# Kernel tuning notes

Hardware: AMD Instinct MI355X
Metric: run time of the kernel (lower is better)

Reference implementation:

```python
import jax, jax.numpy as jnp
import numpy as np

B, S, D, H = 4, 2048, 1024, 16
DK = D // H


def setup_inputs() -> dict:
    key = jax.random.key(0)
    ks = jax.random.split(key, 10)
    std = 0.02
    inp = {
        "input": jax.random.normal(ks[0], (B, S, D), dtype=jnp.float32),
        "attention_reweight": jax.random.uniform(ks[1], (B, S), dtype=jnp.float32),
        "mask": 1,
        "Wq": jax.random.normal(ks[2], (D, D), dtype=jnp.float32) * std,
        "bq": jnp.zeros((D,), dtype=jnp.float32),
        "Wk": jax.random.normal(ks[3], (D, D), dtype=jnp.float32) * std,
        "bk": jnp.zeros((D,), dtype=jnp.float32),
        "Wv": jax.random.normal(ks[4], (D, D), dtype=jnp.float32) * std,
        "bv": jnp.zeros((D,), dtype=jnp.float32),
        "Wo": jax.random.normal(ks[5], (D, D), dtype=jnp.float32) * std,
        "bo": jnp.zeros((D,), dtype=jnp.float32),
    }
    return inp


def reference(input, attention_reweight, mask, Wq, bq, Wk, bk, Wv, bv, Wo, bo):
    b, s, d = input.shape
    # QKV projections (torch Linear: x @ W.T + b)
    q = (input @ Wq.T + bq).reshape(b, s, H, DK).transpose(0, 2, 1, 3)  # [B,H,S,dk]
    k = (input @ Wk.T + bk).reshape(b, s, H, DK).transpose(0, 2, 1, 3)
    v = (input @ Wv.T + bv).reshape(b, s, H, DK).transpose(0, 2, 1, 3)

    scores = jnp.einsum("bhqd,bhkd->bhqk", q, k)  # [B,H,S,S]
    if mask:
        causal = jnp.triu(jnp.ones((s, s), dtype=scores.dtype), k=1)
        scores = scores - causal * 1e9
    scores = scores / jnp.sqrt(jnp.asarray(DK, dtype=jnp.float32))
    # reweight per key position: [B,S] broadcast over heads and query positions
    scores = scores * attention_reweight[:, None, None, :]

    attn = jax.nn.softmax(scores, axis=-1)
    out = jnp.einsum("bhqk,bhkd->bhqd", attn, v)  # [B,H,S,dk]
    out = out.transpose(0, 2, 1, 3).reshape(b, s, d)
    return out @ Wo.T + bo
```

## Files before the change

### kernel.cpp

```cpp
#include <hip/hip_runtime.h>
#include <math.h>

#define B_  4
#define S_  2048
#define D_  1024
#define H_  16
#define DK_ 64

typedef __bf16 bf16x8 __attribute__((ext_vector_type(8)));
typedef float  f32x4  __attribute__((ext_vector_type(4)));

__device__ __forceinline__ unsigned short f2bf(float f) {
  unsigned int u = __builtin_bit_cast(unsigned int, f);
  u += 0x7fffu + ((u >> 16) & 1u);
  return (unsigned short)(u >> 16);
}

__device__ __forceinline__ unsigned short bfbits(float f) {
  __bf16 h = (__bf16)f;
  return __builtin_bit_cast(unsigned short, h);
}

__device__ __forceinline__ f32x4 mfma16(bf16x8 a, bf16x8 b, f32x4 c) {
  return __builtin_amdgcn_mfma_f32_16x16x32_bf16(a, b, c, 0, 0, 0);
}

__device__ __forceinline__ void gl_lds16(const unsigned short* g, unsigned short* l) {
  __builtin_amdgcn_global_load_lds(
      (const __attribute__((address_space(1))) void*)g,
      (__attribute__((address_space(3))) void*)l, 16, 0, 0);
}

__global__ void SAA_cast_all(const float* __restrict__ x,
                             const float* __restrict__ s1, const float* __restrict__ s2,
                             const float* __restrict__ s3, const float* __restrict__ s4,
                             unsigned short* __restrict__ dx,
                             unsigned short* __restrict__ d1, unsigned short* __restrict__ d2,
                             unsigned short* __restrict__ d3, unsigned short* __restrict__ d4)
{
  const int y = blockIdx.y;
  const float* src = (y == 0) ? x : (y == 1) ? s1 : (y == 2) ? s2 : (y == 3) ? s3 : s4;
  unsigned short* dst = (y == 0) ? dx : (y == 1) ? d1 : (y == 2) ? d2 : (y == 3) ? d3 : d4;
  const int n4 = (y == 0) ? (B_ * S_ * D_) / 4 : (D_ * D_) / 4;
  int i = blockIdx.x * blockDim.x + threadIdx.x;
  int stride = gridDim.x * blockDim.x;
  for (; i < n4; i += stride) {
    float4 v = reinterpret_cast<const float4*>(src)[i];
    ushort4 o;
    o.x = f2bf(v.x); o.y = f2bf(v.y); o.z = f2bf(v.z); o.w = f2bf(v.w);
    reinterpret_cast<ushort4*>(dst)[i] = o;
  }
}

__global__ __launch_bounds__(512)
void SAA_gemm_qkv(const unsigned short* __restrict__ Xb,
                  const unsigned short* __restrict__ Wqb,
                  const unsigned short* __restrict__ Wkb,
                  const unsigned short* __restrict__ Wvb,
                  const float* __restrict__ bq,
                  const float* __restrict__ bk,
                  const float* __restrict__ bv,
                  const float* __restrict__ rw,
                  unsigned short* __restrict__ Qo,
                  unsigned short* __restrict__ Ko,
                  unsigned short* __restrict__ Vto)
{
  const int K = D_;
  __shared__ __attribute__((aligned(16))) unsigned short smem[65536];
#define sAp(sl)     (smem + (sl) * 8192)
#define sBp(sl, m)  (smem + 16384 + ((sl) * 3 + (m)) * 8192)

  const int t = threadIdx.x;
  const int w = t >> 6, l = t & 63;
  const int wm = w >> 2, wn = w & 3;
  const int lr = l & 15, lg = l >> 4;
  const int r7 = lr & 7;

  const int bid = blockIdx.x;
  const int m0 = (bid >> 3) * 128;
  const int n0 = (bid & 7) * 128;

  const unsigned short* gA  = Xb  + (size_t)m0 * K;
  const unsigned short* gB0 = Wqb + (size_t)n0 * K;
  const unsigned short* gB1 = Wkb + (size_t)n0 * K;
  const unsigned short* gB2 = Wvb + (size_t)n0 * K;

  int srow[2], soff[2];
#pragma unroll
  for (int i = 0; i < 2; i++) {
    const int c = i * 512 + t;
    srow[i] = c >> 3;
    soff[i] = ((c & 7) ^ (srow[i] & 7)) * 8;
  }

#define STAGE(s, k0)                                                          \
  do {                                                                        \
    _Pragma("unroll")                                                         \
    for (int i = 0; i < 2; i++) {                                             \
      const size_t go = (size_t)srow[i] * K + (k0) + soff[i];                 \
      const int dl = (i * 512 + t) * 8;                                       \
      gl_lds16(gA  + go, sAp(s) + dl);                                        \
      gl_lds16(gB0 + go, sBp(s, 0) + dl);                                     \
      gl_lds16(gB1 + go, sBp(s, 1) + dl);                                     \
      gl_lds16(gB2 + go, sBp(s, 2) + dl);                                     \
    }                                                                         \
  } while (0)

  STAGE(0, 0);

  f32x4 acc[3][4][2] = {};

#pragma unroll 2
  for (int T = 0; T < 16; ++T) {
    __syncthreads();
    if (T + 1 < 16) STAGE((T + 1) & 1, (T + 1) * 64);

    const unsigned short* At = sAp(T & 1);
#pragma unroll
    for (int ks = 0; ks < 2; ++ks) {
      const int swk = (((ks * 4 + lg) ^ r7) << 3);
      bf16x8 afr[4];
#pragma unroll
      for (int mi = 0; mi < 4; ++mi)
        afr[mi] = *reinterpret_cast<const bf16x8*>(
            &At[(wm * 64 + mi * 16 + lr) * 64 + swk]);
#pragma unroll
      for (int mat = 0; mat < 3; ++mat) {
        const unsigned short* Bt = sBp(T & 1, mat);
        bf16x8 bfr[2];
#pragma unroll
        for (int n = 0; n < 2; ++n)
          bfr[n] = *reinterpret_cast<const bf16x8*>(
              &Bt[(wn * 32 + n * 16 + lr) * 64 + swk]);
#pragma unroll
        for (int mi = 0; mi < 4; ++mi)
#pragma unroll
          for (int n = 0; n < 2; ++n)
            acc[mat][mi][n] = mfma16(afr[mi], bfr[n], acc[mat][mi][n]);
      }
    }
  }
#undef STAGE

  __syncthreads();

#pragma unroll
  for (int n = 0; n < 2; ++n) {
    const int col = n0 + wn * 32 + n * 16 + lr;
    const int h = col >> 6, dk = col & 63;
    const float bvv = bv[col];
#pragma unroll
    for (int mi = 0; mi < 4; ++mi) {
      const int row0 = m0 + wm * 64 + mi * 16 + lg * 4;
      const int b = row0 >> 11, s0 = row0 & 2047;
      ushort4 pk;
      pk.x = bfbits(acc[2][mi][n][0] + bvv);
      pk.y = bfbits(acc[2][mi][n][1] + bvv);
      pk.z = bfbits(acc[2][mi][n][2] + bvv);
      pk.w = bfbits(acc[2][mi][n][3] + bvv);
      *reinterpret_cast<ushort4*>(
          &Vto[(((size_t)b * H_ + h) * DK_ + dk) * S_ + s0]) = pk;
    }
  }

  unsigned short* bounce = smem;
  for (int mat = 0; mat < 2; ++mat) {
    const float* bias = mat ? bk : bq;
#pragma unroll
    for (int n = 0; n < 2; ++n) {
      const int col = n0 + wn * 32 + n * 16 + lr;
      const int lcol = wn * 32 + n * 16 + lr;
      const float bs = bias[col];
#pragma unroll
      for (int mi = 0; mi < 4; ++mi) {
#pragma unroll
        for (int r = 0; r < 4; ++r) {
          const int lrow = wm * 64 + mi * 16 + lg * 4 + r;
          float v = acc[mat][mi][n][r] + bs;
          if (mat) v *= 0.18033688011112042f * rw[m0 + lrow];
          bounce[lrow * 132 + lcol] = bfbits(v);
        }
      }
    }
    __syncthreads();
#pragma unroll
    for (int i = 0; i < 2; ++i) {
      const int idx = i * 512 + t;
      const int lrow = idx >> 3, c16 = (idx & 7) * 16;
      const int row = m0 + lrow;
      const int b = row >> 11, s = row & 2047;
      const int col = n0 + c16;
      const int h = col >> 6, dk = col & 63;
      const unsigned short* srcp = &bounce[lrow * 132 + c16];
      unsigned short* dst = (mat ? Ko : Qo) + (((size_t)b * H_ + h) * S_ + s) * DK_ + dk;
#pragma unroll
      for (int j = 0; j < 4; ++j)
        reinterpret_cast<ushort4*>(dst)[j] =
            reinterpret_cast<const ushort4*>(srcp)[j];
    }
    __syncthreads();
  }
#undef sAp
#undef sBp
}

__global__ __launch_bounds__(512)
void SAA_attn(const unsigned short* __restrict__ Q,
              const unsigned short* __restrict__ Kb,
              const unsigned short* __restrict__ Vt,
              const int* __restrict__ maskp,
              unsigned short* __restrict__ Cb)
{
  const int L = (blockIdx.x & 7) * 64 + (blockIdx.x >> 3);
  const int pairid = L & 7;
  const int h = (L >> 3) & 15;
  const int b = L >> 7;

  const int t = threadIdx.x, w = t >> 6, l = t & 63;
  const int lr = l & 15, lg = l >> 4;
  const int mask = maskp[0];

  __shared__ __attribute__((aligned(16))) unsigned short Kt[2][64 * 64];
  __shared__ __attribute__((aligned(16))) unsigned short Vl[2][64 * 64];
  __shared__ __attribute__((aligned(16))) unsigned short Pl[8][16 * 64];

  const size_t bh = (size_t)b * H_ + h;
  const unsigned short* Qbh = Q + bh * S_ * DK_;
  const unsigned short* Kbh = Kb + bh * S_ * DK_;
  const unsigned short* Vbh = Vt + bh * DK_ * S_;
  unsigned short* Pw = &Pl[w][0];

  const int r0 = t >> 3, cc0 = t & 7;
  const int sw0 = (cc0 ^ (r0 & 7)) * 8;

  for (int half = 0; half < 2; ++half) {
    const int qb = half ? (15 - pairid) : pairid;
    const int q0 = qb * 128;
    const int wq = q0 + w * 16;

    bf16x8 qf[2];
#pragma unroll
    for (int ks = 0; ks < 2; ks++)
      qf[ks] = *reinterpret_cast<const bf16x8*>(
          &Qbh[(size_t)(wq + lr) * DK_ + ks * 32 + lg * 8]);

    f32x4 acc[4] = {};
    float lrun[4] = {0.f, 0.f, 0.f, 0.f};

    const int nkt = mask ? (qb * 2 + 2) : (S_ / 64);
    const int wqmax = wq + 15;

    __syncthreads();

    gl_lds16(Kbh + (size_t)r0 * DK_ + sw0, &Kt[0][t * 8]);
    gl_lds16(Vbh + (size_t)r0 * S_ + sw0,  &Vl[0][t * 8]);
    int cur = 0;

    for (int kt = 0; kt < nkt; ++kt) {
      __syncthreads();
      if (kt + 1 < nkt) {
        const int kn = (kt + 1) * 64;
        const int nb = cur ^ 1;
        gl_lds16(Kbh + (size_t)(kn + r0) * DK_ + sw0, &Kt[nb][t * 8]);
        gl_lds16(Vbh + (size_t)r0 * S_ + kn + sw0,    &Vl[nb][t * 8]);
      }

      const int k0 = kt * 64;
      const bool active = (!mask) || (k0 <= wqmax);
      if (active) {
        const unsigned short* Kc = &Kt[cur][0];
        const unsigned short* Vc = &Vl[cur][0];

        __builtin_amdgcn_s_setprio(1);
        f32x4 sc[4] = {};
#pragma unroll
        for (int ks = 0; ks < 2; ++ks) {
          const int swk = (((ks * 4 + lg) ^ (lr & 7)) << 3);
#pragma unroll
          for (int t2 = 0; t2 < 4; ++t2) {
            bf16x8 kf = *reinterpret_cast<const bf16x8*>(&Kc[(t2 * 16 + lr) * 64 + swk]);
            sc[t2] = mfma16(qf[ks], kf, sc[t2]);
          }
        }
        __builtin_amdgcn_s_setprio(0);

        const bool needmask = mask && (k0 + 63 > wq);

#pragma unroll
        for (int r = 0; r < 4; r++) {
          const int row = wq + lg * 4 + r;
          float v0 = sc[0][r], v1 = sc[1][r];
          float v2 = sc[2][r], v3 = sc[3][r];
          if (needmask) {
            if (k0 + lr      > row) v0 = -1e30f;
            if (k0 + 16 + lr > row) v1 = -1e30f;
            if (k0 + 32 + lr > row) v2 = -1e30f;
            if (k0 + 48 + lr > row) v3 = -1e30f;
          }
          const float p0 = __builtin_amdgcn_exp2f(v0);
          const float p1 = __builtin_amdgcn_exp2f(v1);
          const float p2 = __builtin_amdgcn_exp2f(v2);
          const float p3 = __builtin_amdgcn_exp2f(v3);
          lrun[r] += (p0 + p1) + (p2 + p3);
          const int prow = lg * 4 + r;
          const int pr7 = prow & 7;
          const int pbase = prow * 64 + (lr & 7);
          const int hi = lr >> 3;
          Pw[pbase + (((0 + hi) ^ pr7) << 3)] = bfbits(p0);
          Pw[pbase + (((2 + hi) ^ pr7) << 3)] = bfbits(p1);
          Pw[pbase + (((4 + hi) ^ pr7) << 3)] = bfbits(p2);
          Pw[pbase + (((6 + hi) ^ pr7) << 3)] = bfbits(p3);
        }

        __builtin_amdgcn_s_setprio(1);
#pragma unroll
        for (int ks = 0; ks < 2; ++ks) {
          const int swk = (((ks * 4 + lg) ^ (lr & 7)) << 3);
          bf16x8 pf = *reinterpret_cast<const bf16x8*>(&Pw[lr * 64 + swk]);
#pragma unroll
          for (int dt = 0; dt < 4; ++dt) {
            bf16x8 vf = *reinterpret_cast<const bf16x8*>(&Vc[(dt * 16 + lr) * 64 + swk]);
            acc[dt] = mfma16(pf, vf, acc[dt]);
          }
        }
        __builtin_amdgcn_s_setprio(0);
      }
      cur ^= 1;
    }

#pragma unroll
    for (int r = 0; r < 4; r++) {
      float rs = lrun[r];
      rs += __shfl_xor(rs, 1);
      rs += __shfl_xor(rs, 2);
      rs += __shfl_xor(rs, 4);
      rs += __shfl_xor(rs, 8);
      lrun[r] = __builtin_amdgcn_rcpf(rs);
    }
#pragma unroll
    for (int dt = 0; dt < 4; dt++) {
#pragma unroll
      for (int r = 0; r < 4; r++) {
        const int row = wq + lg * 4 + r;
        const int col = h * DK_ + dt * 16 + lr;
        Cb[((size_t)b * S_ + row) * D_ + col] = bfbits(acc[dt][r] * lrun[r]);
      }
    }
  }
}

__global__ __launch_bounds__(512)
void SAA_gemm_out(const unsigned short* __restrict__ Cb,
                  const unsigned short* __restrict__ Wob,
                  const float* __restrict__ bo,
                  float* __restrict__ Y)
{
  const int K = D_;
  __shared__ __attribute__((aligned(16))) unsigned short lA[2][512 * 64];
  __shared__ __attribute__((aligned(16))) unsigned short lB[2][64 * 64];

  const int L = (blockIdx.x & 7) * 32 + (blockIdx.x >> 3);
  const int nx = L & 15, my = L >> 4;

  const int t = threadIdx.x;
  const int w = t >> 6, l = t & 63;
  const int lr = l & 15, lg = l >> 4;
  const int r7 = lr & 7;

  const int m0 = my * 512;
  const int n0 = nx * 64;

  const unsigned short* gA = Cb + (size_t)m0 * K;
  const unsigned short* gB = Wob + (size_t)n0 * K;

  const int sr = t >> 3;
  const int soff = ((t & 7) ^ (sr & 7)) * 8;

#define STAGEO(s, k0)                                                         \
  do {                                                                        \
    _Pragma("unroll")                                                         \
    for (int i = 0; i < 8; i++)                                               \
      gl_lds16(gA + (size_t)(i * 64 + sr) * K + (k0) + soff,                  \
               &lA[s][(i * 512 + t) * 8]);                                    \
    gl_lds16(gB + (size_t)sr * K + (k0) + soff, &lB[s][t * 8]);               \
  } while (0)

  STAGEO(0, 0);

  f32x4 acc[4][4] = {};

#pragma unroll 2
  for (int T = 0; T < 16; ++T) {
    __syncthreads();
    if (T + 1 < 16) STAGEO((T + 1) & 1, (T + 1) * 64);

    const unsigned short* At = lA[T & 1];
    const unsigned short* Bt = lB[T & 1];
#pragma unroll
    for (int ks = 0; ks < 2; ks++) {
      const int swk = (((ks * 4 + lg) ^ r7) << 3);
      bf16x8 af[4], bfr[4];
#pragma unroll
      for (int i = 0; i < 4; i++)
        af[i] = *reinterpret_cast<const bf16x8*>(&At[(w * 64 + i * 16 + lr) * 64 + swk]);
#pragma unroll
      for (int j = 0; j < 4; j++)
        bfr[j] = *reinterpret_cast<const bf16x8*>(&Bt[(j * 16 + lr) * 64 + swk]);
#pragma unroll
      for (int i = 0; i < 4; i++)
#pragma unroll
        for (int j = 0; j < 4; j++)
          acc[i][j] = mfma16(af[i], bfr[j], acc[i][j]);
    }
  }
#undef STAGEO

#pragma unroll
  for (int j = 0; j < 4; j++) {
    const int col = n0 + j * 16 + lr;
    const float bsv = bo[col];
#pragma unroll
    for (int i = 0; i < 4; i++) {
#pragma unroll
      for (int r = 0; r < 4; r++) {
        const int row = m0 + w * 64 + i * 16 + lg * 4 + r;
        Y[(size_t)row * D_ + col] = acc[i][j][r] + bsv;
      }
    }
  }
}

extern "C" void kernel_launch(void* const* d_in, const int* in_sizes, int n_in,
                              void* d_out, int out_size, void* d_ws, size_t ws_size,
                              hipStream_t stream) {
  const float* input = (const float*)d_in[0];
  const float* rw    = (const float*)d_in[1];
  const int*   maskp = (const int*)d_in[2];
  const float* Wq = (const float*)d_in[3];
  const float* bq = (const float*)d_in[4];
  const float* Wk = (const float*)d_in[5];
  const float* bk = (const float*)d_in[6];
  const float* Wv = (const float*)d_in[7];
  const float* bv = (const float*)d_in[8];
  const float* Wo = (const float*)d_in[9];
  const float* bo = (const float*)d_in[10];

  char* ws = (char*)d_ws;
  unsigned short* Xb  = (unsigned short*)(ws);
  unsigned short* Wqb = (unsigned short*)(ws + (16u << 20));
  unsigned short* Wkb = (unsigned short*)(ws + (18u << 20));
  unsigned short* Wvb = (unsigned short*)(ws + (20u << 20));
  unsigned short* Wob = (unsigned short*)(ws + (22u << 20));
  unsigned short* Qo  = (unsigned short*)(ws + (24u << 20));
  unsigned short* Ko  = (unsigned short*)(ws + (40u << 20));
  unsigned short* Vto = (unsigned short*)(ws + (56u << 20));
  unsigned short* Cb  = Xb;

  SAA_cast_all<<<dim3(512, 5), 256, 0, stream>>>(input, Wq, Wk, Wv, Wo,
                                                 Xb, Wqb, Wkb, Wvb, Wob);

  SAA_gemm_qkv<<<512, 512, 0, stream>>>(Xb, Wqb, Wkb, Wvb, bq, bk, bv, rw,
                                        Qo, Ko, Vto);
  SAA_attn<<<512, 512, 0, stream>>>(Qo, Ko, Vto, maskp, Cb);
  SAA_gemm_out<<<256, 512, 0, stream>>>(Cb, Wob, bo, (float*)d_out);
}
```

Measured before the change: 171.3 us.

## Fuse fp32-to-bf16 cast of input activations into QKV GEMM A-tile loading

Removes the separate conversion of the large input tensor to bf16. The QKV GEMM now loads fp32 A tiles into registers, converts them, and writes swizzled bf16 into LDS after the MFMA compute of the current tile. This saves a full write and re-read of the activation buffer. In exchange, the GEMM reads twice the bytes for A from global memory across its n-blocks and uses extra registers for the staged loads.

```diff
diff --git a/kernel.cpp b/kernel.cpp
--- a/kernel.cpp
+++ b/kernel.cpp
@@ -31,17 +31,22 @@
       (__attribute__((address_space(3))) void*)l, 16, 0, 0);
 }
 
-__global__ void SAA_cast_all(const float* __restrict__ x,
-                             const float* __restrict__ s1, const float* __restrict__ s2,
-                             const float* __restrict__ s3, const float* __restrict__ s4,
-                             unsigned short* __restrict__ dx,
-                             unsigned short* __restrict__ d1, unsigned short* __restrict__ d2,
-                             unsigned short* __restrict__ d3, unsigned short* __restrict__ d4)
+__device__ __forceinline__ bf16x8 pack8(float4 a, float4 b) {
+  bf16x8 r;
+  r[0] = (__bf16)a.x; r[1] = (__bf16)a.y; r[2] = (__bf16)a.z; r[3] = (__bf16)a.w;
+  r[4] = (__bf16)b.x; r[5] = (__bf16)b.y; r[6] = (__bf16)b.z; r[7] = (__bf16)b.w;
+  return r;
+}
+
+__global__ void SAA_cast4(const float* __restrict__ s0, const float* __restrict__ s1,
+                          const float* __restrict__ s2, const float* __restrict__ s3,
+                          unsigned short* __restrict__ d0, unsigned short* __restrict__ d1,
+                          unsigned short* __restrict__ d2, unsigned short* __restrict__ d3)
 {
   const int y = blockIdx.y;
-  const float* src = (y == 0) ? x : (y == 1) ? s1 : (y == 2) ? s2 : (y == 3) ? s3 : s4;
-  unsigned short* dst = (y == 0) ? dx : (y == 1) ? d1 : (y == 2) ? d2 : (y == 3) ? d3 : d4;
-  const int n4 = (y == 0) ? (B_ * S_ * D_) / 4 : (D_ * D_) / 4;
+  const float* src = (y == 0) ? s0 : (y == 1) ? s1 : (y == 2) ? s2 : s3;
+  unsigned short* dst = (y == 0) ? d0 : (y == 1) ? d1 : (y == 2) ? d2 : d3;
+  const int n4 = (D_ * D_) / 4;
   int i = blockIdx.x * blockDim.x + threadIdx.x;
   int stride = gridDim.x * blockDim.x;
   for (; i < n4; i += stride) {
@@ -53,7 +58,7 @@
 }
 
 __global__ __launch_bounds__(512)
-void SAA_gemm_qkv(const unsigned short* __restrict__ Xb,
+void SAA_gemm_qkv(const float* __restrict__ Xf,
                   const unsigned short* __restrict__ Wqb,
                   const unsigned short* __restrict__ Wkb,
                   const unsigned short* __restrict__ Wvb,
@@ -80,7 +85,7 @@
   const int m0 = (bid >> 3) * 128;
   const int n0 = (bid & 7) * 128;
 
-  const unsigned short* gA  = Xb  + (size_t)m0 * K;
+  const float* gA = Xf + (size_t)m0 * K;
   const unsigned short* gB0 = Wqb + (size_t)n0 * K;
   const unsigned short* gB1 = Wkb + (size_t)n0 * K;
   const unsigned short* gB2 = Wvb + (size_t)n0 * K;
@@ -93,27 +98,48 @@
     soff[i] = ((c & 7) ^ (srow[i] & 7)) * 8;
   }
 
-#define STAGE(s, k0)                                                          \
+  float4 a4[2][2];
+
+#define LOADA(k0)                                                             \
+  do {                                                                        \
+    _Pragma("unroll")                                                         \
+    for (int i = 0; i < 2; i++) {                                             \
+      const float* p = gA + (size_t)srow[i] * K + (k0) + soff[i];             \
+      a4[i][0] = *reinterpret_cast<const float4*>(p);                         \
+      a4[i][1] = *reinterpret_cast<const float4*>(p + 4);                     \
+    }                                                                         \
+  } while (0)
+
+#define WRITEA(s)                                                             \
+  do {                                                                        \
+    _Pragma("unroll")                                                         \
+    for (int i = 0; i < 2; i++)                                               \
+      *reinterpret_cast<bf16x8*>(sAp(s) + (i * 512 + t) * 8) =                \
+          pack8(a4[i][0], a4[i][1]);                                          \
+  } while (0)
+
+#define STAGEB(s, k0)                                                         \
   do {                                                                        \
     _Pragma("unroll")                                                         \
     for (int i = 0; i < 2; i++) {                                             \
       const size_t go = (size_t)srow[i] * K + (k0) + soff[i];                 \
       const int dl = (i * 512 + t) * 8;                                       \
-      gl_lds16(gA  + go, sAp(s) + dl);                                        \
       gl_lds16(gB0 + go, sBp(s, 0) + dl);                                     \
       gl_lds16(gB1 + go, sBp(s, 1) + dl);                                     \
       gl_lds16(gB2 + go, sBp(s, 2) + dl);                                     \
     }                                                                         \
   } while (0)
 
-  STAGE(0, 0);
+  LOADA(0);
+  STAGEB(0, 0);
+  WRITEA(0);
 
   f32x4 acc[3][4][2] = {};
 
 #pragma unroll 2
   for (int T = 0; T < 16; ++T) {
     __syncthreads();
-    if (T + 1 < 16) STAGE((T + 1) & 1, (T + 1) * 64);
+    if (T + 1 < 16) { LOADA((T + 1) * 64); STAGEB((T + 1) & 1, (T + 1) * 64); }
 
     const unsigned short* At = sAp(T & 1);
 #pragma unroll
@@ -139,8 +165,12 @@
             acc[mat][mi][n] = mfma16(afr[mi], bfr[n], acc[mat][mi][n]);
       }
     }
-  }
-#undef STAGE
+
+    if (T + 1 < 16) WRITEA((T + 1) & 1);
+  }
+#undef LOADA
+#undef WRITEA
+#undef STAGEB
 
   __syncthreads();
 
@@ -456,10 +486,9 @@
   unsigned short* Vto = (unsigned short*)(ws + (56u << 20));
   unsigned short* Cb  = Xb;
 
-  SAA_cast_all<<<dim3(512, 5), 256, 0, stream>>>(input, Wq, Wk, Wv, Wo,
-                                                 Xb, Wqb, Wkb, Wvb, Wob);
-
-  SAA_gemm_qkv<<<512, 512, 0, stream>>>(Xb, Wqb, Wkb, Wvb, bq, bk, bv, rw,
+  SAA_cast4<<<dim3(512, 4), 256, 0, stream>>>(Wq, Wk, Wv, Wo, Wqb, Wkb, Wvb, Wob);
+
+  SAA_gemm_qkv<<<512, 512, 0, stream>>>(input, Wqb, Wkb, Wvb, bq, bk, bv, rw,
                                         Qo, Ko, Vto);
   SAA_attn<<<512, 512, 0, stream>>>(Qo, Ko, Vto, maskp, Cb);
   SAA_gemm_out<<<256, 512, 0, stream>>>(Cb, Wob, bo, (float*)d_out);
```

Result: faster. 167.5 us (-2.2%).
